# Performance work log

Measured on AMD Instinct MI355X. Metric: run time of the kernel, lower is better.

Reference implementation:

```python
import jax, jax.numpy as jnp
import numpy as np

IN_DIM = 128
HIDDEN = 256
OUT_DIM = 128
N_NODES = 100000
N_EDGES = 500000
N_MC = 2


def setup_inputs() -> dict:
    key = jax.random.key(0)
    k1, k2, k3, k4 = jax.random.split(key, 4)
    edge_index = jax.random.randint(k1, (2, N_EDGES), 0, N_NODES, dtype=jnp.int64)
    mc_embeddings = jax.random.normal(k2, (N_MC, N_NODES, IN_DIM), dtype=jnp.float32)
    # kaiming_normal for Linear1 (fan_in = 2*IN_DIM) and Linear2 (fan_in = HIDDEN)
    W1 = jax.random.normal(k3, (2 * IN_DIM, HIDDEN), dtype=jnp.float32) * np.sqrt(2.0 / (2 * IN_DIM))
    b1 = jnp.zeros((HIDDEN,), dtype=jnp.float32)
    W2 = jax.random.normal(k4, (HIDDEN, OUT_DIM), dtype=jnp.float32) * np.sqrt(2.0 / HIDDEN)
    b2 = jnp.zeros((OUT_DIM,), dtype=jnp.float32)
    return {"edge_index": edge_index, "mc_embeddings": mc_embeddings,
            "W1": W1, "b1": b1, "W2": W2, "b2": b2}


def reference(edge_index, mc_embeddings, W1, b1, W2, b2):
    # cat([x[src], x[dst]]) @ W1 == x[src] @ W1[:D] + x[dst] @ W1[D:]
    src, dst = edge_index[0], edge_index[1]
    W1a, W1b = W1[:IN_DIM], W1[IN_DIM:]  # [D, H] each

    def per_mc(x):  # x: [N, D]
        h = x[src] @ W1a + x[dst] @ W1b + b1          # [E, H]
        h = jax.nn.relu(h)
        return h @ W2 + b2                            # [E, out]

    return jax.vmap(per_mc)(mc_embeddings)           # [M, E, out]
```

## Files before the change

### kernel.cpp

```cpp
#include <hip/hip_runtime.h>
#include <hip/hip_bf16.h>

#define IN_DIM   128
#define HIDDEN   256
#define OUT_DIM  128
#define N_NODES  100000
#define N_EDGES  500000
#define N_ROWS   (2 * N_EDGES)

typedef __bf16 bf16x8 __attribute__((ext_vector_type(8)));
typedef float  f32x4  __attribute__((ext_vector_type(4)));

#define W1S_OFF 0
#define W2S_OFF 131072

__global__ void prep_weights(const float* __restrict__ W1,
                             const float* __restrict__ W2,
                             unsigned char* __restrict__ ws) {
  int t = blockIdx.x * 256 + threadIdx.x;
  if (t < HIDDEN * HIDDEN) {
    int n = t & 255, k = t >> 8;
    __bf16 b = (__bf16)W1[k * HIDDEN + n];
    int byte = W1S_OFF + n * 512 + ((k * 2) ^ ((n & 7) << 4));
    *reinterpret_cast<__bf16*>(ws + byte) = b;
  } else {
    int t2 = t - HIDDEN * HIDDEN;
    if (t2 < HIDDEN * OUT_DIM) {
      int n = t2 & 127, k = t2 >> 7;
      __bf16 b = (__bf16)W2[k * OUT_DIM + n];
      int byte = W2S_OFF + n * 512 + ((k * 2) ^ ((n & 7) << 4));
      *reinterpret_cast<__bf16*>(ws + byte) = b;
    }
  }
}

static __device__ __forceinline__ unsigned pack_bf16(float a, float b) {
  __bf16 x = (__bf16)a, y = (__bf16)b;
  unsigned short ux = __builtin_bit_cast(unsigned short, x);
  unsigned short uy = __builtin_bit_cast(unsigned short, y);
  return (unsigned)ux | ((unsigned)uy << 16);
}

__global__ __launch_bounds__(256, 4)
void edge_mlp(const int* __restrict__ eidx,
              const float* __restrict__ x,
              const float* __restrict__ b1,
              const float* __restrict__ b2,
              const unsigned char* __restrict__ ws,
              float* __restrict__ out) {
  __shared__ __align__(16) unsigned char wbuf[2][8192];

  const int tid  = threadIdx.x;
  const int wv   = tid >> 6;
  const int lane = tid & 63;
  const int l15  = lane & 15;
  const int lk   = lane >> 4;

  const long base = (long)blockIdx.x * 64;
  const long gr   = base + wv * 16 + l15;
  const int  mc   = (gr >= N_EDGES) ? 1 : 0;
  const int  e    = (int)(gr - (long)mc * N_EDGES);
  const int  sn   = eidx[e];
  const int  dn   = eidx[N_EDGES + e];
  const float* xs = x + ((long)mc * N_NODES + sn) * IN_DIM;
  const float* xd = x + ((long)mc * N_NODES + dn) * IN_DIM;

  bf16x8 a1[8];
#pragma unroll
  for (int kt = 0; kt < 8; ++kt) {
    int k = kt * 32 + lk * 8;
    const float* p = (k < IN_DIM) ? (xs + k) : (xd + (k - IN_DIM));
    float4 f0 = *reinterpret_cast<const float4*>(p);
    float4 f1 = *reinterpret_cast<const float4*>(p + 4);
    bf16x8 a;
    a[0] = (__bf16)f0.x; a[1] = (__bf16)f0.y; a[2] = (__bf16)f0.z; a[3] = (__bf16)f0.w;
    a[4] = (__bf16)f1.x; a[5] = (__bf16)f1.y; a[6] = (__bf16)f1.z; a[7] = (__bf16)f1.w;
    a1[kt] = a;
  }

#define STAGE(t, buf)                                                          \
  do {                                                                         \
    const unsigned char* g_ = ws + (t) * 8192;                                 \
    __builtin_amdgcn_global_load_lds(                                          \
        (const __attribute__((address_space(1))) unsigned int*)(g_ + tid * 16),\
        (__attribute__((address_space(3))) unsigned int*)(&wbuf[buf][tid * 16]),\
        16, 0, 0);                                                             \
    __builtin_amdgcn_global_load_lds(                                          \
        (const __attribute__((address_space(1))) unsigned int*)(g_ + 4096 + tid * 16), \
        (__attribute__((address_space(3))) unsigned int*)(&wbuf[buf][4096 + tid * 16]), \
        16, 0, 0);                                                             \
  } while (0)

  STAGE(0, 0);
  __syncthreads();

  const int swz  = (l15 & 7) << 4;
  const int rowb = l15 * 512;
  const int s0   = (lk & 1) * 32 + l15;
  const int s1   = s0 + 16;
  const bool hi  = (lk >= 2);

  bf16x8 a2[8];
  unsigned pe0 = 0, pe1 = 0;

#pragma unroll
  for (int c = 0; c < 16; ++c) {
    STAGE(c + 1, (c + 1) & 1);
    f32x4 acc = (f32x4){0.f, 0.f, 0.f, 0.f};
#pragma unroll
    for (int kt = 0; kt < 8; ++kt) {
      bf16x8 wf = *reinterpret_cast<const bf16x8*>(
          &wbuf[c & 1][rowb + ((kt * 64 + lk * 16) ^ swz)]);
      acc = __builtin_amdgcn_mfma_f32_16x16x32_bf16(wf, a1[kt], acc, 0, 0, 0);
    }
    float4 bv = *reinterpret_cast<const float4*>(b1 + c * 16 + lk * 4);
    unsigned p0 = pack_bf16(fmaxf(acc[0] + bv.x, 0.f), fmaxf(acc[1] + bv.y, 0.f));
    unsigned p1 = pack_bf16(fmaxf(acc[2] + bv.z, 0.f), fmaxf(acc[3] + bv.w, 0.f));
    if ((c & 1) == 0) {
      pe0 = p0; pe1 = p1;
    } else {
      unsigned A0 = (unsigned)__shfl((int)pe0, s0), A1 = (unsigned)__shfl((int)pe1, s0);
      unsigned A2 = (unsigned)__shfl((int)pe0, s1), A3 = (unsigned)__shfl((int)pe1, s1);
      unsigned B0 = (unsigned)__shfl((int)p0, s0),  B1 = (unsigned)__shfl((int)p1, s0);
      unsigned B2 = (unsigned)__shfl((int)p0, s1),  B3 = (unsigned)__shfl((int)p1, s1);
      uint4 w;
      w.x = hi ? B0 : A0; w.y = hi ? B1 : A1;
      w.z = hi ? B2 : A2; w.w = hi ? B3 : A3;
      a2[c >> 1] = __builtin_bit_cast(bf16x8, w);
    }
    __syncthreads();
  }

#pragma unroll
  for (int c2 = 0; c2 < 8; ++c2) {
    const int t = 16 + c2;
    if (t + 1 < 24) STAGE(t + 1, (t + 1) & 1);
    f32x4 acc = (f32x4){0.f, 0.f, 0.f, 0.f};
#pragma unroll
    for (int kt = 0; kt < 8; ++kt) {
      bf16x8 bf = *reinterpret_cast<const bf16x8*>(
          &wbuf[t & 1][rowb + ((kt * 64 + lk * 16) ^ swz)]);
      acc = __builtin_amdgcn_mfma_f32_16x16x32_bf16(a2[kt], bf, acc, 0, 0, 0);
    }
    float bv2 = b2[c2 * 16 + l15];
    const long r0 = base + wv * 16 + lk * 4;
#pragma unroll
    for (int r = 0; r < 4; ++r)
      out[(r0 + r) * OUT_DIM + c2 * 16 + l15] = acc[r] + bv2;
    if (c2 < 7) __syncthreads();
  }
#undef STAGE
}

extern "C" void kernel_launch(void* const* d_in, const int* in_sizes, int n_in,
                              void* d_out, int out_size, void* d_ws, size_t ws_size,
                              hipStream_t stream) {
  const int*   eidx = (const int*)d_in[0];
  const float* x    = (const float*)d_in[1];
  const float* b1   = (const float*)d_in[3];
  const float* b2   = (const float*)d_in[5];
  float* out = (float*)d_out;
  unsigned char* ws = (unsigned char*)d_ws;

  prep_weights<<<(HIDDEN * HIDDEN + HIDDEN * OUT_DIM) / 256, 256, 0, stream>>>(
      (const float*)d_in[2], (const float*)d_in[4], ws);

  edge_mlp<<<N_ROWS / 64, 256, 0, stream>>>(eidx, x, b1, b2, ws, out);
  (void)in_sizes; (void)n_in; (void)out_size; (void)ws_size;
}
```

Measured before the change: 386.3 us.

## Switch edge MLP to 32x32x16 MFMA tiles with 128-thread blocks

Moves both GEMM stages from 16x16x32 to 32x32x16 bf16 MFMA, so each wave now owns 32 edges and blocks shrink to two waves covering 64 rows. The hidden-activation re-layout between layers uses v_permlane32_swap instead of eight lane shuffles, and weight staging chunks double to 16 KB with half as many barriers. Larger MFMA tiles raise arithmetic per LDS weight read but double per-lane registers (16-wide accumulators, 16-entry A arrays), which may reduce occupancy. The occupancy hint in launch_bounds is dropped.

```diff
diff --git a/kernel.cpp b/kernel.cpp
--- a/kernel.cpp
+++ b/kernel.cpp
@@ -8,8 +8,8 @@
 #define N_EDGES  500000
 #define N_ROWS   (2 * N_EDGES)
 
-typedef __bf16 bf16x8 __attribute__((ext_vector_type(8)));
-typedef float  f32x4  __attribute__((ext_vector_type(4)));
+typedef __bf16 bf16x8  __attribute__((ext_vector_type(8)));
+typedef float  f32x16  __attribute__((ext_vector_type(16)));
 
 #define W1S_OFF 0
 #define W2S_OFF 131072
@@ -41,23 +41,23 @@
   return (unsigned)ux | ((unsigned)uy << 16);
 }
 
-__global__ __launch_bounds__(256, 4)
+__global__ __launch_bounds__(128)
 void edge_mlp(const int* __restrict__ eidx,
               const float* __restrict__ x,
               const float* __restrict__ b1,
               const float* __restrict__ b2,
               const unsigned char* __restrict__ ws,
               float* __restrict__ out) {
-  __shared__ __align__(16) unsigned char wbuf[2][8192];
+  __shared__ __align__(16) unsigned char wbuf[2][16384];
 
   const int tid  = threadIdx.x;
   const int wv   = tid >> 6;
   const int lane = tid & 63;
-  const int l15  = lane & 15;
-  const int lk   = lane >> 4;
+  const int el   = lane & 31;
+  const int hi   = lane >> 5;
 
   const long base = (long)blockIdx.x * 64;
-  const long gr   = base + wv * 16 + l15;
+  const long gr   = base + wv * 32 + el;
   const int  mc   = (gr >= N_EDGES) ? 1 : 0;
   const int  e    = (int)(gr - (long)mc * N_EDGES);
   const int  sn   = eidx[e];
@@ -65,89 +65,91 @@
   const float* xs = x + ((long)mc * N_NODES + sn) * IN_DIM;
   const float* xd = x + ((long)mc * N_NODES + dn) * IN_DIM;
 
-  bf16x8 a1[8];
+  bf16x8 a1[16];
 #pragma unroll
-  for (int kt = 0; kt < 8; ++kt) {
-    int k = kt * 32 + lk * 8;
-    const float* p = (k < IN_DIM) ? (xs + k) : (xd + (k - IN_DIM));
+  for (int s = 0; s < 16; ++s) {
+    int k0 = s * 16 + hi * 8;
+    const float* p = (s < 8) ? (xs + k0) : (xd + (k0 - IN_DIM));
     float4 f0 = *reinterpret_cast<const float4*>(p);
     float4 f1 = *reinterpret_cast<const float4*>(p + 4);
     bf16x8 a;
     a[0] = (__bf16)f0.x; a[1] = (__bf16)f0.y; a[2] = (__bf16)f0.z; a[3] = (__bf16)f0.w;
     a[4] = (__bf16)f1.x; a[5] = (__bf16)f1.y; a[6] = (__bf16)f1.z; a[7] = (__bf16)f1.w;
-    a1[kt] = a;
+    a1[s] = a;
   }
 
-#define STAGE(t, buf)                                                          \
+#define STAGE(t, b)                                                            \
   do {                                                                         \
-    const unsigned char* g_ = ws + (t) * 8192;                                 \
-    __builtin_amdgcn_global_load_lds(                                          \
-        (const __attribute__((address_space(1))) unsigned int*)(g_ + tid * 16),\
-        (__attribute__((address_space(3))) unsigned int*)(&wbuf[buf][tid * 16]),\
-        16, 0, 0);                                                             \
-    __builtin_amdgcn_global_load_lds(                                          \
-        (const __attribute__((address_space(1))) unsigned int*)(g_ + 4096 + tid * 16), \
-        (__attribute__((address_space(3))) unsigned int*)(&wbuf[buf][4096 + tid * 16]), \
-        16, 0, 0);                                                             \
+    const unsigned char* g_ = ws + (t) * 16384;                                \
+    _Pragma("unroll")                                                          \
+    for (int i_ = 0; i_ < 8; ++i_) {                                           \
+      __builtin_amdgcn_global_load_lds(                                        \
+          (const __attribute__((address_space(1))) unsigned int*)(g_ + i_ * 2048 + tid * 16), \
+          (__attribute__((address_space(3))) unsigned int*)(&wbuf[b][i_ * 2048 + tid * 16]),  \
+          16, 0, 0);                                                           \
+    }                                                                          \
   } while (0)
 
   STAGE(0, 0);
   __syncthreads();
 
-  const int swz  = (l15 & 7) << 4;
-  const int rowb = l15 * 512;
-  const int s0   = (lk & 1) * 32 + l15;
-  const int s1   = s0 + 16;
-  const bool hi  = (lk >= 2);
+  const int rowb = el * 512;
+  const int swz  = (el & 7) << 4;
 
-  bf16x8 a2[8];
-  unsigned pe0 = 0, pe1 = 0;
+  bf16x8 a2[16];
 
 #pragma unroll
-  for (int c = 0; c < 16; ++c) {
-    STAGE(c + 1, (c + 1) & 1);
-    f32x4 acc = (f32x4){0.f, 0.f, 0.f, 0.f};
+  for (int cc = 0; cc < 8; ++cc) {
+    STAGE(cc + 1, (cc + 1) & 1);
+    f32x16 acc = {};
 #pragma unroll
-    for (int kt = 0; kt < 8; ++kt) {
+    for (int ks = 0; ks < 16; ++ks) {
       bf16x8 wf = *reinterpret_cast<const bf16x8*>(
-          &wbuf[c & 1][rowb + ((kt * 64 + lk * 16) ^ swz)]);
-      acc = __builtin_amdgcn_mfma_f32_16x16x32_bf16(wf, a1[kt], acc, 0, 0, 0);
+          &wbuf[cc & 1][rowb + ((ks * 32 + hi * 16) ^ swz)]);
+      acc = __builtin_amdgcn_mfma_f32_32x32x16_bf16(wf, a1[ks], acc, 0, 0, 0);
     }
-    float4 bv = *reinterpret_cast<const float4*>(b1 + c * 16 + lk * 4);
-    unsigned p0 = pack_bf16(fmaxf(acc[0] + bv.x, 0.f), fmaxf(acc[1] + bv.y, 0.f));
-    unsigned p1 = pack_bf16(fmaxf(acc[2] + bv.z, 0.f), fmaxf(acc[3] + bv.w, 0.f));
-    if ((c & 1) == 0) {
-      pe0 = p0; pe1 = p1;
-    } else {
-      unsigned A0 = (unsigned)__shfl((int)pe0, s0), A1 = (unsigned)__shfl((int)pe1, s0);
-      unsigned A2 = (unsigned)__shfl((int)pe0, s1), A3 = (unsigned)__shfl((int)pe1, s1);
-      unsigned B0 = (unsigned)__shfl((int)p0, s0),  B1 = (unsigned)__shfl((int)p1, s0);
-      unsigned B2 = (unsigned)__shfl((int)p0, s1),  B3 = (unsigned)__shfl((int)p1, s1);
-      uint4 w;
-      w.x = hi ? B0 : A0; w.y = hi ? B1 : A1;
-      w.z = hi ? B2 : A2; w.w = hi ? B3 : A3;
-      a2[c >> 1] = __builtin_bit_cast(bf16x8, w);
-    }
+    float4 bv0 = *reinterpret_cast<const float4*>(b1 + cc * 32 + hi * 4);
+    float4 bv1 = *reinterpret_cast<const float4*>(b1 + cc * 32 + 8 + hi * 4);
+    float4 bv2 = *reinterpret_cast<const float4*>(b1 + cc * 32 + 16 + hi * 4);
+    float4 bv3 = *reinterpret_cast<const float4*>(b1 + cc * 32 + 24 + hi * 4);
+    unsigned w0 = pack_bf16(fmaxf(acc[0] + bv0.x, 0.f),  fmaxf(acc[1] + bv0.y, 0.f));
+    unsigned w1 = pack_bf16(fmaxf(acc[2] + bv0.z, 0.f),  fmaxf(acc[3] + bv0.w, 0.f));
+    unsigned w2 = pack_bf16(fmaxf(acc[4] + bv1.x, 0.f),  fmaxf(acc[5] + bv1.y, 0.f));
+    unsigned w3 = pack_bf16(fmaxf(acc[6] + bv1.z, 0.f),  fmaxf(acc[7] + bv1.w, 0.f));
+    unsigned w4 = pack_bf16(fmaxf(acc[8] + bv2.x, 0.f),  fmaxf(acc[9] + bv2.y, 0.f));
+    unsigned w5 = pack_bf16(fmaxf(acc[10] + bv2.z, 0.f), fmaxf(acc[11] + bv2.w, 0.f));
+    unsigned w6 = pack_bf16(fmaxf(acc[12] + bv3.x, 0.f), fmaxf(acc[13] + bv3.y, 0.f));
+    unsigned w7 = pack_bf16(fmaxf(acc[14] + bv3.z, 0.f), fmaxf(acc[15] + bv3.w, 0.f));
+    asm("v_permlane32_swap_b32 %0, %1" : "+v"(w0), "+v"(w2));
+    asm("v_permlane32_swap_b32 %0, %1" : "+v"(w1), "+v"(w3));
+    asm("v_permlane32_swap_b32 %0, %1" : "+v"(w4), "+v"(w6));
+    asm("v_permlane32_swap_b32 %0, %1" : "+v"(w5), "+v"(w7));
+    uint4 fe; fe.x = w0; fe.y = w1; fe.z = w2; fe.w = w3;
+    uint4 fo; fo.x = w4; fo.y = w5; fo.z = w6; fo.w = w7;
+    a2[2 * cc]     = __builtin_bit_cast(bf16x8, fe);
+    a2[2 * cc + 1] = __builtin_bit_cast(bf16x8, fo);
     __syncthreads();
   }
 
 #pragma unroll
-  for (int c2 = 0; c2 < 8; ++c2) {
-    const int t = 16 + c2;
-    if (t + 1 < 24) STAGE(t + 1, (t + 1) & 1);
-    f32x4 acc = (f32x4){0.f, 0.f, 0.f, 0.f};
+  for (int oc = 0; oc < 4; ++oc) {
+    const int t = 8 + oc;
+    if (t + 1 < 12) STAGE(t + 1, (t + 1) & 1);
+    f32x16 acc = {};
 #pragma unroll
-    for (int kt = 0; kt < 8; ++kt) {
-      bf16x8 bf = *reinterpret_cast<const bf16x8*>(
-          &wbuf[t & 1][rowb + ((kt * 64 + lk * 16) ^ swz)]);
-      acc = __builtin_amdgcn_mfma_f32_16x16x32_bf16(a2[kt], bf, acc, 0, 0, 0);
+    for (int kk = 0; kk < 16; ++kk) {
+      bf16x8 wf = *reinterpret_cast<const bf16x8*>(
+          &wbuf[t & 1][rowb + ((kk * 32 + hi * 16) ^ swz)]);
+      acc = __builtin_amdgcn_mfma_f32_32x32x16_bf16(a2[kk], wf, acc, 0, 0, 0);
     }
-    float bv2 = b2[c2 * 16 + l15];
-    const long r0 = base + wv * 16 + lk * 4;
+    float bvo = b2[oc * 32 + el];
+    const long r0 = base + wv * 32;
 #pragma unroll
-    for (int r = 0; r < 4; ++r)
-      out[(r0 + r) * OUT_DIM + c2 * 16 + l15] = acc[r] + bv2;
-    if (c2 < 7) __syncthreads();
+    for (int reg = 0; reg < 16; ++reg) {
+      int m = (reg & 3) + 8 * (reg >> 2) + 4 * hi;
+      out[(r0 + m) * OUT_DIM + oc * 32 + el] = acc[reg] + bvo;
+    }
+    if (oc < 3) __syncthreads();
   }
 #undef STAGE
 }
@@ -165,6 +167,6 @@
   prep_weights<<<(HIDDEN * HIDDEN + HIDDEN * OUT_DIM) / 256, 256, 0, stream>>>(
       (const float*)d_in[2], (const float*)d_in[4], ws);
 
-  edge_mlp<<<N_ROWS / 64, 256, 0, stream>>>(eidx, x, b1, b2, ws, out);
+  edge_mlp<<<N_ROWS / 64, 128, 0, stream>>>(eidx, x, b1, b2, ws, out);
   (void)in_sizes; (void)n_in; (void)out_size; (void)ws_size;
 }
```

After: 359.4 us. 1.07x faster.
